# Optimization experiments

Measured on AMD Instinct MI355X. Metric: run time of the kernel, lower is better.

The kernel has to match this reference:

```python
import jax, jax.numpy as jnp
import numpy as np

N_S = 50000
N_T = 50000
D_IN = 256
D_OUT = 128
E = 1600000


def setup_inputs() -> dict:
    key = jax.random.key(0)
    ks = jax.random.split(key, 7)
    inp_s = jax.random.normal(ks[0], (N_S, D_IN), dtype=jnp.float32)
    inp_t = jax.random.normal(ks[1], (N_T, D_IN), dtype=jnp.float32)
    adj_s_idx = jax.random.randint(ks[2], (E, 2), 0, N_S, dtype=jnp.int32)
    adj_s_val = jax.random.uniform(ks[3], (E,), dtype=jnp.float32)
    adj_t_idx = jax.random.randint(ks[4], (E, 2), 0, N_T, dtype=jnp.int32)
    adj_t_val = jax.random.uniform(ks[5], (E,), dtype=jnp.float32)
    # Glorot-uniform shared weights, as in weight_variable_glorot
    init_range = np.sqrt(6.0 / (D_IN + D_OUT))
    W = jax.random.uniform(ks[6], (D_IN, D_OUT), minval=-init_range,
                           maxval=init_range, dtype=jnp.float32)
    return {"inp_s": inp_s, "inp_t": inp_t,
            "adj_s_idx": adj_s_idx, "adj_s_val": adj_s_val,
            "adj_t_idx": adj_t_idx, "adj_t_val": adj_t_val,
            "W": W}


def _spmm(idx, val, x, n_rows):
    # sparse [n_rows, n_cols] @ dense x: gather source rows, scale, scatter-add to dest
    rows, cols = idx[:, 0], idx[:, 1]
    msgs = x[cols] * val[:, None]                      # [E, D_OUT]
    return jax.ops.segment_sum(msgs, rows, num_segments=n_rows)


def _gcn_branch(x, idx, val, W, n_rows):
    # dropout = 0.0 -> identity; dense GEMM -> SpMM -> relu
    h = x @ W                                          # [N, D_OUT]
    h = _spmm(idx, val, h, n_rows)
    return jax.nn.relu(h)


def reference(inp_s, inp_t, adj_s_idx, adj_s_val, adj_t_idx, adj_t_val, W):
    out_s = _gcn_branch(inp_s, adj_s_idx, adj_s_val, W, N_S)
    out_t = _gcn_branch(inp_t, adj_t_idx, adj_t_val, W, N_T)
    return (out_s, out_t)
```

## Files before the change

kernel.cpp:

```cpp
#include <hip/hip_runtime.h>
#include <cstdint>
#include <cstddef>

#define D_IN   256
#define D_OUT  128
#define NB_MAX 256
#define KV_CAP 12288
#define NCB    8

typedef short bf16x8 __attribute__((ext_vector_type(8)));
typedef float f32x4  __attribute__((ext_vector_type(4)));

union Frag { bf16x8 v; uint32_t u[4]; };

struct Branch {
  const float* X;
  const int*   idx;
  const float* val;
  uint16_t* H;
  int*   ptr;
  int*   bucketCur;
  uint64_t* kv2;
  uint32_t* csr4;
  float* out;
};

__device__ inline uint32_t cvt_pk_bf16(float lo, float hi) {
  uint32_t r;
  asm("v_cvt_pk_bf16_f32 %0, %1, %2" : "=v"(r) : "v"(lo), "v"(hi));
  return r;
}

__device__ inline int block_scan256_excl(int v, int tid) {
  int lane = tid & 63, w = tid >> 6;
  int s = v;
  #pragma unroll
  for (int off = 1; off < 64; off <<= 1) {
    int t = __shfl_up(s, off);
    if (lane >= off) s += t;
  }
  __shared__ int wsum[4];
  if (lane == 63) wsum[w] = s;
  __syncthreads();
  int add = 0;
  #pragma unroll
  for (int i = 0; i < 4; ++i) add += (i < w) ? wsum[i] : 0;
  return s + add - v;
}

__global__ __launch_bounds__(256) void wprep3_kernel(const float* __restrict__ W,
                                                     uint16_t* __restrict__ WT3) {
  int n = blockIdx.x;
  int t = threadIdx.x;
  int ks = t >> 5, g = (t >> 3) & 3, j = t & 7;
  int k = ks * 32 + ((j < 4) ? (4 * g + j) : (16 + 4 * g + (j - 4)));
  uint32_t u = __float_as_uint(W[k * 128 + n]);
  WT3[(size_t)((ks * 4 + g) * 128 + n) * 8 + j] =
      (uint16_t)((u + 0x7FFFu + ((u >> 16) & 1u)) >> 16);
}

__global__ __launch_bounds__(256, 3) void bin_gemm_kernel(const uint16_t* __restrict__ WT3,
                                                          Branch b0, Branch b1,
                                                          int n_rows, int ne, int nb) {
  Branch b = blockIdx.y ? b1 : b0;
  const int t = threadIdx.x;
  __shared__ uint8_t smem[32768];

  if (blockIdx.z == 0) {
    int* hist  = (int*)smem;
    int* lcur  = hist + NB_MAX;
    int* gbase = lcur + NB_MAX;
    const int base = blockIdx.x * 4096;
    if (base >= ne) return;
    if (t < nb) hist[t] = 0;
    __syncthreads();
    uint64_t kv2[16];
    int bkt[16];
    #pragma unroll
    for (int i = 0; i < 16; ++i) {
      int e = base + i * 256 + t;
      bkt[i] = -1;
      if (e < ne) {
        int2 rc = ((const int2*)b.idx)[e];
        uint32_t v = __float_as_uint(b.val[e]);
        kv2[i] = ((uint64_t)v << 32) | ((uint32_t)rc.x << 16) | (uint32_t)rc.y;
        bkt[i] = rc.x >> 8;
        atomicAdd(&hist[bkt[i]], 1);
      }
    }
    __syncthreads();
    if (t < nb) {
      int h = hist[t];
      gbase[t] = h ? atomicAdd(&b.bucketCur[t], h) : 0;
      lcur[t] = 0;
    }
    __syncthreads();
    #pragma unroll
    for (int i = 0; i < 16; ++i) {
      if (bkt[i] >= 0) {
        int pos = gbase[bkt[i]] + atomicAdd(&lcur[bkt[i]], 1);
        if (pos < KV_CAP)
          b.kv2[(size_t)bkt[i] * KV_CAP + pos] = kv2[i];
      }
    }
    return;
  }

  const int w = t >> 6, l = t & 63;
  const int c = l & 15, g = l >> 4;
  const int row0 = blockIdx.x * 128;
  if (row0 >= n_rows) return;

  auto stage = [&](int ks, int buf) {
    #pragma unroll
    for (int i = 0; i < 4; ++i) {
      int row = i * 32 + (t >> 3);
      int gr = row0 + row; if (gr > n_rows - 1) gr = n_rows - 1;
      int kb = ((t & 7) * 16) ^ ((row & 7) << 4);
      const float* src = b.X + (size_t)gr * D_IN + ks * 32 + (kb >> 2);
      __builtin_amdgcn_global_load_lds(
          (const __attribute__((address_space(1))) uint32_t*)src,
          (__attribute__((address_space(3))) uint32_t*)&smem[buf * 16384 + i * 4096 + t * 16],
          16, 0, 0);
    }
  };

  const uint4* Bp = (const uint4*)WT3;

  f32x4 acc[2][8];
  #pragma unroll
  for (int i = 0; i < 2; ++i)
    #pragma unroll
    for (int j = 0; j < 8; ++j) acc[i][j] = (f32x4){0.f, 0.f, 0.f, 0.f};

  stage(0, 0);
  asm volatile("s_waitcnt vmcnt(0)" ::: "memory");
  __syncthreads();

  for (int ks = 0; ks < 8; ++ks) {
    int buf = ks & 1;
    uint4 bu[8];
    #pragma unroll
    for (int nf = 0; nf < 8; ++nf)
      bu[nf] = Bp[(ks * 4 + g) * 128 + nf * 16 + c];
    if (ks < 7) stage(ks + 1, buf ^ 1);

    Frag A[2];
    #pragma unroll
    for (int rf = 0; rf < 2; ++rf) {
      int row = w * 32 + rf * 16 + c;
      const uint8_t* base = &smem[buf * 16384 + row * 128];
      int swz = (row & 7) << 4;
      float4 x0 = *(const float4*)(base + ((g * 16) ^ swz));
      float4 x1 = *(const float4*)(base + ((64 + g * 16) ^ swz));
      A[rf].u[0] = cvt_pk_bf16(x0.x, x0.y);
      A[rf].u[1] = cvt_pk_bf16(x0.z, x0.w);
      A[rf].u[2] = cvt_pk_bf16(x1.x, x1.y);
      A[rf].u[3] = cvt_pk_bf16(x1.z, x1.w);
    }

    #pragma unroll
    for (int nf = 0; nf < 8; ++nf) {
      Frag B;
      B.u[0] = bu[nf].x; B.u[1] = bu[nf].y; B.u[2] = bu[nf].z; B.u[3] = bu[nf].w;
      acc[0][nf] = __builtin_amdgcn_mfma_f32_16x16x32_bf16(A[0].v, B.v, acc[0][nf], 0, 0, 0);
      acc[1][nf] = __builtin_amdgcn_mfma_f32_16x16x32_bf16(A[1].v, B.v, acc[1][nf], 0, 0, 0);
    }

    if (ks < 7) {
      asm volatile("s_waitcnt vmcnt(0)" ::: "memory");
      __syncthreads();
    }
  }

  #pragma unroll
  for (int rf = 0; rf < 2; ++rf)
    #pragma unroll
    for (int nf = 0; nf < 8; ++nf)
      #pragma unroll
      for (int r = 0; r < 4; ++r) {
        float v = acc[rf][nf][r];
        float o = __shfl_xor(v, 1);
        uint32_t pk = cvt_pk_bf16(v, o);
        uint32_t pk2 = __shfl_xor(pk, 2);
        int row_g = row0 + w * 32 + rf * 16 + 4 * g + r;
        if ((c & 3) == 0 && row_g < n_rows) {
          uint2 d; d.x = pk; d.y = pk2;
          *(uint2*)(b.H + (size_t)row_g * D_OUT + nf * 16 + c) = d;
        }
      }
}

__global__ __launch_bounds__(256) void bucket_csr_kernel(Branch b0, Branch b1, int n, int nb) {
  Branch b = blockIdx.y ? b1 : b0;
  const int bkt = blockIdx.x;
  const int tid = threadIdx.x;
  __shared__ int sbase[NB_MAX];
  __shared__ int hist2[256 * NCB];
  __shared__ int cur2[256 * NCB];

  int cntv = (tid < nb) ? b.bucketCur[tid] : 0;
  if (cntv > KV_CAP) cntv = KV_CAP;
  int excl0 = block_scan256_excl(cntv, tid);
  if (tid < nb) sbase[tid] = excl0;
  if (bkt == 0 && tid == nb - 1) b.ptr[n] = excl0 + cntv;
  __syncthreads();

  const int dstBase = sbase[bkt];
  int cnt = b.bucketCur[bkt];
  if (cnt > KV_CAP) cnt = KV_CAP;
  const uint64_t* src = b.kv2 + (size_t)bkt * KV_CAP;

  #pragma unroll
  for (int i = 0; i < NCB; ++i) hist2[i * 256 + tid] = 0;
  __syncthreads();
  for (int e = tid; e < cnt; e += 256) {
    uint64_t kv = src[e];
    int lr = (int)((kv >> 16) & 0xFF);
    int cb = (int)(kv & 0xFFFFu) >> 13;
    atomicAdd(&hist2[lr * NCB + cb], 1);
  }
  __syncthreads();

  int h[NCB], rowtot = 0;
  #pragma unroll
  for (int j = 0; j < NCB; ++j) { h[j] = hist2[tid * NCB + j]; rowtot += h[j]; }
  int rowExcl = block_scan256_excl(rowtot, tid);
  int row = bkt * 256 + tid;
  if (row < n) b.ptr[row] = dstBase + rowExcl;
  int run = dstBase + rowExcl;
  #pragma unroll
  for (int j = 0; j < NCB; ++j) { cur2[tid * NCB + j] = run; run += h[j]; }
  __syncthreads();

  for (int e = tid; e < cnt; e += 256) {
    uint64_t kv = src[e];
    int lr = (int)((kv >> 16) & 0xFF);
    uint32_t col = (uint32_t)(kv & 0xFFFFu);
    int cb = (int)col >> 13;
    uint32_t u = (uint32_t)(kv >> 32);
    uint32_t vbf = (u + 0x7FFFu + ((u >> 16) & 1u)) & 0xFFFF0000u;
    int pos = atomicAdd(&cur2[lr * NCB + cb], 1);
    b.csr4[pos] = vbf | col;
  }
}

__global__ __launch_bounds__(256) void gather_kernel(Branch b0, Branch b1, int n_rows) {
  const int bid = blockIdx.x;
  const int br  = (bid & 7) >> 2;
  const int local = (bid >> 3) * 4 + (bid & 3);
  Branch b = br ? b1 : b0;
  int row = local * 16 + (threadIdx.x >> 4);
  if (row >= n_rows) return;
  int lane4 = threadIdx.x & 15;
  const uint4* Hq = (const uint4*)b.H;
  int beg = b.ptr[row], end = b.ptr[row + 1];
  float4 acc0 = make_float4(0.f, 0.f, 0.f, 0.f);
  float4 acc1 = make_float4(0.f, 0.f, 0.f, 0.f);

  auto fma_h = [&](uint32_t k, uint4 h) {
    float v = __uint_as_float(k & 0xFFFF0000u);
    float f0 = __uint_as_float(h.x << 16), f1 = __uint_as_float(h.x & 0xFFFF0000u);
    float f2 = __uint_as_float(h.y << 16), f3 = __uint_as_float(h.y & 0xFFFF0000u);
    float f4 = __uint_as_float(h.z << 16), f5 = __uint_as_float(h.z & 0xFFFF0000u);
    float f6 = __uint_as_float(h.w << 16), f7 = __uint_as_float(h.w & 0xFFFF0000u);
    acc0.x = fmaf(f0, v, acc0.x); acc0.y = fmaf(f1, v, acc0.y);
    acc0.z = fmaf(f2, v, acc0.z); acc0.w = fmaf(f3, v, acc0.w);
    acc1.x = fmaf(f4, v, acc1.x); acc1.y = fmaf(f5, v, acc1.y);
    acc1.z = fmaf(f6, v, acc1.z); acc1.w = fmaf(f7, v, acc1.w);
  };

  int e = beg;
  for (; e + 8 <= end; e += 8) {
    uint32_t k[8];
    #pragma unroll
    for (int i = 0; i < 8; ++i) k[i] = b.csr4[e + i];
    uint4 h[8];
    #pragma unroll
    for (int i = 0; i < 8; ++i)
      h[i] = Hq[(size_t)(k[i] & 0xFFFFu) * 16 + lane4];
    #pragma unroll
    for (int i = 0; i < 8; ++i) fma_h(k[i], h[i]);
  }
  for (; e < end; ++e) {
    uint32_t k = b.csr4[e];
    uint4 h = Hq[(size_t)(k & 0xFFFFu) * 16 + lane4];
    fma_h(k, h);
  }

  float4 o0, o1;
  o0.x = fmaxf(acc0.x, 0.f); o0.y = fmaxf(acc0.y, 0.f);
  o0.z = fmaxf(acc0.z, 0.f); o0.w = fmaxf(acc0.w, 0.f);
  o1.x = fmaxf(acc1.x, 0.f); o1.y = fmaxf(acc1.y, 0.f);
  o1.z = fmaxf(acc1.z, 0.f); o1.w = fmaxf(acc1.w, 0.f);
  float* orow = b.out + (size_t)row * D_OUT + lane4 * 8;
  *(float4*)orow = o0;
  *(float4*)(orow + 4) = o1;
}

extern "C" void kernel_launch(void* const* d_in, const int* in_sizes, int n_in,
                              void* d_out, int out_size, void* d_ws, size_t ws_size,
                              hipStream_t stream) {
  const float* inp_s = (const float*)d_in[0];
  const float* inp_t = (const float*)d_in[1];
  const int*   idx_s = (const int*)d_in[2];
  const float* val_s = (const float*)d_in[3];
  const int*   idx_t = (const int*)d_in[4];
  const float* val_t = (const float*)d_in[5];
  const float* W     = (const float*)d_in[6];
  float* out = (float*)d_out;

  const int n  = in_sizes[0] / D_IN;
  const int ne = in_sizes[3];
  const int nb = (n + 255) >> 8;

  char* p = (char*)d_ws;
  auto alloc = [&](size_t bytes) -> char* {
    char* r = p;
    p += (bytes + 255) & ~(size_t)255;
    return r;
  };
  uint16_t* H_s    = (uint16_t*)alloc((size_t)n * D_OUT * 2);
  uint16_t* H_t    = (uint16_t*)alloc((size_t)n * D_OUT * 2);
  uint16_t* WT3    = (uint16_t*)alloc((size_t)128 * 256 * 2);
  int* ptr_s       = (int*)alloc((size_t)(n + 1) * 4);
  int* ptr_t       = (int*)alloc((size_t)(n + 1) * 4);
  int* bcur        = (int*)alloc((size_t)2 * NB_MAX * 4);
  int* bcur_s      = bcur;
  int* bcur_t      = bcur + NB_MAX;
  uint64_t* kv2_s  = (uint64_t*)alloc((size_t)NB_MAX * KV_CAP * 8);
  uint64_t* kv2_t  = (uint64_t*)alloc((size_t)NB_MAX * KV_CAP * 8);
  uint32_t* c4_s   = (uint32_t*)alloc((size_t)ne * 4);
  uint32_t* c4_t   = (uint32_t*)alloc((size_t)ne * 4);

  Branch bs = { inp_s, idx_s, val_s, H_s, ptr_s, bcur_s, kv2_s, c4_s, out };
  Branch bt = { inp_t, idx_t, val_t, H_t, ptr_t, bcur_t, kv2_t, c4_t,
                out + (size_t)n * D_OUT };

  const int nblkE = (ne + 4095) / 4096;
  const int nblkG = (n + 127) / 128;
  const int nblkF = nblkE > nblkG ? nblkE : nblkG;
  const int bpb   = (((n + 15) / 16) + 3) & ~3;

  hipMemsetAsync(bcur, 0, (size_t)2 * NB_MAX * 4, stream);
  wprep3_kernel<<<dim3(128), 256, 0, stream>>>(W, WT3);
  bin_gemm_kernel<<<dim3(nblkF, 2, 2), 256, 0, stream>>>(WT3, bs, bt, n, ne, nb);
  bucket_csr_kernel<<<dim3(nb, 2), 256, 0, stream>>>(bs, bt, n, nb);
  gather_kernel<<<dim3(2 * bpb), 256, 0, stream>>>(bs, bt, n);
}
```

Measured before the change: 196.2 us.

## Split H into column segments and run gather in four column passes

The GEMM epilogue now writes H in a segmented layout, four 32-column slabs of 64 bytes per row each. The single gather kernel is replaced by four launches, each covering one slab. The aim is to shrink the randomly accessed H working set per pass (about 3.2 MB per branch) so it fits in L2 or the infinity cache and random row gathers hit cache. The cost is reading the CSR indices four times, four launches, and narrower 8-byte loads per lane.

```diff
diff --git a/kernel.cpp b/kernel.cpp
--- a/kernel.cpp
+++ b/kernel.cpp
@@ -7,6 +7,8 @@
 #define NB_MAX 256
 #define KV_CAP 12288
 #define NCB    8
+#define NPASS  4
+#define SEGW   32
 
 typedef short bf16x8 __attribute__((ext_vector_type(8)));
 typedef float f32x4  __attribute__((ext_vector_type(4)));
@@ -185,8 +187,10 @@
         uint32_t pk2 = __shfl_xor(pk, 2);
         int row_g = row0 + w * 32 + rf * 16 + 4 * g + r;
         if ((c & 3) == 0 && row_g < n_rows) {
+          int seg = nf >> 1;
+          int cip = (nf & 1) * 16 + c;
           uint2 d; d.x = pk; d.y = pk2;
-          *(uint2*)(b.H + (size_t)row_g * D_OUT + nf * 16 + c) = d;
+          *(uint2*)(b.H + (size_t)seg * n_rows * SEGW + (size_t)row_g * SEGW + cip) = d;
         }
       }
 }
@@ -245,29 +249,25 @@
   }
 }
 
-__global__ __launch_bounds__(256) void gather_kernel(Branch b0, Branch b1, int n_rows) {
+__global__ __launch_bounds__(256) void gather_pass_kernel(Branch b0, Branch b1, int n_rows,
+                                                          int pass) {
   const int bid = blockIdx.x;
   const int br  = (bid & 7) >> 2;
   const int local = (bid >> 3) * 4 + (bid & 3);
   Branch b = br ? b1 : b0;
-  int row = local * 16 + (threadIdx.x >> 4);
+  int row = local * 32 + (threadIdx.x >> 3);
   if (row >= n_rows) return;
-  int lane4 = threadIdx.x & 15;
-  const uint4* Hq = (const uint4*)b.H;
+  int lane8 = threadIdx.x & 7;
+  const uint16_t* Hp = b.H + (size_t)pass * n_rows * SEGW;
   int beg = b.ptr[row], end = b.ptr[row + 1];
-  float4 acc0 = make_float4(0.f, 0.f, 0.f, 0.f);
-  float4 acc1 = make_float4(0.f, 0.f, 0.f, 0.f);
-
-  auto fma_h = [&](uint32_t k, uint4 h) {
+  float4 acc = make_float4(0.f, 0.f, 0.f, 0.f);
+
+  auto fma_h = [&](uint32_t k, uint2 h) {
     float v = __uint_as_float(k & 0xFFFF0000u);
     float f0 = __uint_as_float(h.x << 16), f1 = __uint_as_float(h.x & 0xFFFF0000u);
     float f2 = __uint_as_float(h.y << 16), f3 = __uint_as_float(h.y & 0xFFFF0000u);
-    float f4 = __uint_as_float(h.z << 16), f5 = __uint_as_float(h.z & 0xFFFF0000u);
-    float f6 = __uint_as_float(h.w << 16), f7 = __uint_as_float(h.w & 0xFFFF0000u);
-    acc0.x = fmaf(f0, v, acc0.x); acc0.y = fmaf(f1, v, acc0.y);
-    acc0.z = fmaf(f2, v, acc0.z); acc0.w = fmaf(f3, v, acc0.w);
-    acc1.x = fmaf(f4, v, acc1.x); acc1.y = fmaf(f5, v, acc1.y);
-    acc1.z = fmaf(f6, v, acc1.z); acc1.w = fmaf(f7, v, acc1.w);
+    acc.x = fmaf(f0, v, acc.x); acc.y = fmaf(f1, v, acc.y);
+    acc.z = fmaf(f2, v, acc.z); acc.w = fmaf(f3, v, acc.w);
   };
 
   int e = beg;
@@ -275,27 +275,23 @@
     uint32_t k[8];
     #pragma unroll
     for (int i = 0; i < 8; ++i) k[i] = b.csr4[e + i];
-    uint4 h[8];
+    uint2 h[8];
     #pragma unroll
     for (int i = 0; i < 8; ++i)
-      h[i] = Hq[(size_t)(k[i] & 0xFFFFu) * 16 + lane4];
+      h[i] = *(const uint2*)(Hp + (size_t)(k[i] & 0xFFFFu) * SEGW + lane8 * 4);
     #pragma unroll
     for (int i = 0; i < 8; ++i) fma_h(k[i], h[i]);
   }
   for (; e < end; ++e) {
     uint32_t k = b.csr4[e];
-    uint4 h = Hq[(size_t)(k & 0xFFFFu) * 16 + lane4];
+    uint2 h = *(const uint2*)(Hp + (size_t)(k & 0xFFFFu) * SEGW + lane8 * 4);
     fma_h(k, h);
   }
 
-  float4 o0, o1;
-  o0.x = fmaxf(acc0.x, 0.f); o0.y = fmaxf(acc0.y, 0.f);
-  o0.z = fmaxf(acc0.z, 0.f); o0.w = fmaxf(acc0.w, 0.f);
-  o1.x = fmaxf(acc1.x, 0.f); o1.y = fmaxf(acc1.y, 0.f);
-  o1.z = fmaxf(acc1.z, 0.f); o1.w = fmaxf(acc1.w, 0.f);
-  float* orow = b.out + (size_t)row * D_OUT + lane4 * 8;
-  *(float4*)orow = o0;
-  *(float4*)(orow + 4) = o1;
+  float4 o;
+  o.x = fmaxf(acc.x, 0.f); o.y = fmaxf(acc.y, 0.f);
+  o.z = fmaxf(acc.z, 0.f); o.w = fmaxf(acc.w, 0.f);
+  *(float4*)&b.out[(size_t)row * D_OUT + pass * SEGW + lane8 * 4] = o;
 }
 
 extern "C" void kernel_launch(void* const* d_in, const int* in_sizes, int n_in,
@@ -340,11 +336,12 @@
   const int nblkE = (ne + 4095) / 4096;
   const int nblkG = (n + 127) / 128;
   const int nblkF = nblkE > nblkG ? nblkE : nblkG;
-  const int bpb   = (((n + 15) / 16) + 3) & ~3;
+  const int bpb   = (((n + 31) / 32) + 3) & ~3;
 
   hipMemsetAsync(bcur, 0, (size_t)2 * NB_MAX * 4, stream);
   wprep3_kernel<<<dim3(128), 256, 0, stream>>>(W, WT3);
   bin_gemm_kernel<<<dim3(nblkF, 2, 2), 256, 0, stream>>>(WT3, bs, bt, n, ne, nb);
   bucket_csr_kernel<<<dim3(nb, 2), 256, 0, stream>>>(bs, bt, n, nb);
-  gather_kernel<<<dim3(2 * bpb), 256, 0, stream>>>(bs, bt, n);
-}
+  for (int pass = 0; pass < NPASS; ++pass)
+    gather_pass_kernel<<<dim3(2 * bpb), 256, 0, stream>>>(bs, bt, n, pass);
+}
```

Result: slower. 218.1 us (+11.2%).

## Split bin/GEMM kernel and deepen GEMM load pipeline to four LDS stages

Applied to the files above, without the earlier changes.

The fused binning+GEMM kernel is split into two separate launches. The GEMM now uses a four-buffer LDS ring (64KB) with A tiles prefetched three steps ahead and B fragments two steps ahead. It waits with partial vmcnt counts instead of draining all loads every iteration. This is meant to hide global-load latency in the GEMM. The cost is more LDS per block, which lowers occupancy, plus an extra kernel launch and no more overlap between the binning and GEMM work.

```diff
diff --git a/kernel.cpp b/kernel.cpp
--- a/kernel.cpp
+++ b/kernel.cpp
@@ -59,57 +59,57 @@
       (uint16_t)((u + 0x7FFFu + ((u >> 16) & 1u)) >> 16);
 }
 
-__global__ __launch_bounds__(256, 3) void bin_gemm_kernel(const uint16_t* __restrict__ WT3,
-                                                          Branch b0, Branch b1,
-                                                          int n_rows, int ne, int nb) {
+__global__ __launch_bounds__(256) void bin_kernel(Branch b0, Branch b1, int ne, int nb) {
+  Branch b = blockIdx.y ? b1 : b0;
+  __shared__ int hist[NB_MAX];
+  __shared__ int lcur[NB_MAX];
+  __shared__ int gbase[NB_MAX];
+  const int t = threadIdx.x;
+  const int base = blockIdx.x * 4096;
+  if (base >= ne) return;
+  if (t < nb) hist[t] = 0;
+  __syncthreads();
+  uint64_t kv2[16];
+  int bkt[16];
+  #pragma unroll
+  for (int i = 0; i < 16; ++i) {
+    int e = base + i * 256 + t;
+    bkt[i] = -1;
+    if (e < ne) {
+      int2 rc = ((const int2*)b.idx)[e];
+      uint32_t v = __float_as_uint(b.val[e]);
+      kv2[i] = ((uint64_t)v << 32) | ((uint32_t)rc.x << 16) | (uint32_t)rc.y;
+      bkt[i] = rc.x >> 8;
+      atomicAdd(&hist[bkt[i]], 1);
+    }
+  }
+  __syncthreads();
+  if (t < nb) {
+    int h = hist[t];
+    gbase[t] = h ? atomicAdd(&b.bucketCur[t], h) : 0;
+    lcur[t] = 0;
+  }
+  __syncthreads();
+  #pragma unroll
+  for (int i = 0; i < 16; ++i) {
+    if (bkt[i] >= 0) {
+      int pos = gbase[bkt[i]] + atomicAdd(&lcur[bkt[i]], 1);
+      if (pos < KV_CAP)
+        b.kv2[(size_t)bkt[i] * KV_CAP + pos] = kv2[i];
+    }
+  }
+}
+
+__global__ __launch_bounds__(256) void gemm_kernel(const uint16_t* __restrict__ WT3,
+                                                   Branch b0, Branch b1, int n_rows) {
   Branch b = blockIdx.y ? b1 : b0;
   const int t = threadIdx.x;
-  __shared__ uint8_t smem[32768];
-
-  if (blockIdx.z == 0) {
-    int* hist  = (int*)smem;
-    int* lcur  = hist + NB_MAX;
-    int* gbase = lcur + NB_MAX;
-    const int base = blockIdx.x * 4096;
-    if (base >= ne) return;
-    if (t < nb) hist[t] = 0;
-    __syncthreads();
-    uint64_t kv2[16];
-    int bkt[16];
-    #pragma unroll
-    for (int i = 0; i < 16; ++i) {
-      int e = base + i * 256 + t;
-      bkt[i] = -1;
-      if (e < ne) {
-        int2 rc = ((const int2*)b.idx)[e];
-        uint32_t v = __float_as_uint(b.val[e]);
-        kv2[i] = ((uint64_t)v << 32) | ((uint32_t)rc.x << 16) | (uint32_t)rc.y;
-        bkt[i] = rc.x >> 8;
-        atomicAdd(&hist[bkt[i]], 1);
-      }
-    }
-    __syncthreads();
-    if (t < nb) {
-      int h = hist[t];
-      gbase[t] = h ? atomicAdd(&b.bucketCur[t], h) : 0;
-      lcur[t] = 0;
-    }
-    __syncthreads();
-    #pragma unroll
-    for (int i = 0; i < 16; ++i) {
-      if (bkt[i] >= 0) {
-        int pos = gbase[bkt[i]] + atomicAdd(&lcur[bkt[i]], 1);
-        if (pos < KV_CAP)
-          b.kv2[(size_t)bkt[i] * KV_CAP + pos] = kv2[i];
-      }
-    }
-    return;
-  }
-
   const int w = t >> 6, l = t & 63;
   const int c = l & 15, g = l >> 4;
   const int row0 = blockIdx.x * 128;
   if (row0 >= n_rows) return;
+
+  __shared__ uint8_t sX[4][16384];
 
   auto stage = [&](int ks, int buf) {
     #pragma unroll
@@ -120,12 +120,18 @@
       const float* src = b.X + (size_t)gr * D_IN + ks * 32 + (kb >> 2);
       __builtin_amdgcn_global_load_lds(
           (const __attribute__((address_space(1))) uint32_t*)src,
-          (__attribute__((address_space(3))) uint32_t*)&smem[buf * 16384 + i * 4096 + t * 16],
+          (__attribute__((address_space(3))) uint32_t*)&sX[buf][i * 4096 + t * 16],
           16, 0, 0);
     }
   };
 
   const uint4* Bp = (const uint4*)WT3;
+  uint4 bu[2][8];
+  auto loadB = [&](int ks, int set) {
+    #pragma unroll
+    for (int nf = 0; nf < 8; ++nf)
+      bu[set][nf] = Bp[(ks * 4 + g) * 128 + nf * 16 + c];
+  };
 
   f32x4 acc[2][8];
   #pragma unroll
@@ -134,22 +140,23 @@
     for (int j = 0; j < 8; ++j) acc[i][j] = (f32x4){0.f, 0.f, 0.f, 0.f};
 
   stage(0, 0);
-  asm volatile("s_waitcnt vmcnt(0)" ::: "memory");
-  __syncthreads();
-
+  loadB(0, 0);
+  stage(1, 1);
+  loadB(1, 1);
+  stage(2, 2);
+
+  #pragma unroll
   for (int ks = 0; ks < 8; ++ks) {
-    int buf = ks & 1;
-    uint4 bu[8];
-    #pragma unroll
-    for (int nf = 0; nf < 8; ++nf)
-      bu[nf] = Bp[(ks * 4 + g) * 128 + nf * 16 + c];
-    if (ks < 7) stage(ks + 1, buf ^ 1);
+    if (ks < 6)       asm volatile("s_waitcnt vmcnt(16)" ::: "memory");
+    else if (ks == 6) asm volatile("s_waitcnt vmcnt(12)" ::: "memory");
+    else              asm volatile("s_waitcnt vmcnt(0)"  ::: "memory");
+    __builtin_amdgcn_s_barrier();
 
     Frag A[2];
     #pragma unroll
     for (int rf = 0; rf < 2; ++rf) {
       int row = w * 32 + rf * 16 + c;
-      const uint8_t* base = &smem[buf * 16384 + row * 128];
+      const uint8_t* base = &sX[ks & 3][row * 128];
       int swz = (row & 7) << 4;
       float4 x0 = *(const float4*)(base + ((g * 16) ^ swz));
       float4 x1 = *(const float4*)(base + ((64 + g * 16) ^ swz));
@@ -162,15 +169,14 @@
     #pragma unroll
     for (int nf = 0; nf < 8; ++nf) {
       Frag B;
-      B.u[0] = bu[nf].x; B.u[1] = bu[nf].y; B.u[2] = bu[nf].z; B.u[3] = bu[nf].w;
+      B.u[0] = bu[ks & 1][nf].x; B.u[1] = bu[ks & 1][nf].y;
+      B.u[2] = bu[ks & 1][nf].z; B.u[3] = bu[ks & 1][nf].w;
       acc[0][nf] = __builtin_amdgcn_mfma_f32_16x16x32_bf16(A[0].v, B.v, acc[0][nf], 0, 0, 0);
       acc[1][nf] = __builtin_amdgcn_mfma_f32_16x16x32_bf16(A[1].v, B.v, acc[1][nf], 0, 0, 0);
     }
 
-    if (ks < 7) {
-      asm volatile("s_waitcnt vmcnt(0)" ::: "memory");
-      __syncthreads();
-    }
+    if (ks < 6) loadB(ks + 2, ks & 1);
+    if (ks < 5) stage(ks + 3, (ks + 3) & 3);
   }
 
   #pragma unroll
@@ -339,12 +345,12 @@
 
   const int nblkE = (ne + 4095) / 4096;
   const int nblkG = (n + 127) / 128;
-  const int nblkF = nblkE > nblkG ? nblkE : nblkG;
   const int bpb   = (((n + 15) / 16) + 3) & ~3;
 
   hipMemsetAsync(bcur, 0, (size_t)2 * NB_MAX * 4, stream);
   wprep3_kernel<<<dim3(128), 256, 0, stream>>>(W, WT3);
-  bin_gemm_kernel<<<dim3(nblkF, 2, 2), 256, 0, stream>>>(WT3, bs, bt, n, ne, nb);
+  bin_kernel<<<dim3(nblkE, 2), 256, 0, stream>>>(bs, bt, ne, nb);
+  gemm_kernel<<<dim3(nblkG, 2), 256, 0, stream>>>(WT3, bs, bt, n);
   bucket_csr_kernel<<<dim3(nb, 2), 256, 0, stream>>>(bs, bt, n, nb);
   gather_kernel<<<dim3(2 * bpb), 256, 0, stream>>>(bs, bt, n);
 }
```

Result: slower. 200.6 us (+2.2%).
